# Kernel optimization log

Hardware: AMD Instinct MI355X
Metric: run time of the kernel (lower is better)

## Reference

```python
import jax, jax.numpy as jnp
import numpy as np

BS, NA, HW, C, HEADS = 16, 256, 1024, 512, 8
FEAT_RES = 32  # hw = feat_res**2


def setup_inputs() -> dict:
    key = jax.random.key(0)
    ks = jax.random.split(key, 16)

    def lin_w(k, din, dout):
        return (jax.random.normal(k, (din, dout), jnp.float32) / np.sqrt(din)).astype(jnp.float32)

    inp = {
        "tok_agent": jax.random.normal(ks[0], (BS, NA, C), jnp.float32),
        "enc_feat_supp": jax.random.normal(ks[1], (BS, HW, C), jnp.float32),
        "enc_feat_query": jax.random.normal(ks[2], (BS, HW, C), jnp.float32),
        # projection weights stored as [in, out]
        "W_qa": lin_w(ks[3], C, C), "b_qa": jnp.zeros((C,), jnp.float32),
        "W_ks": lin_w(ks[4], C, C), "b_ks": jnp.zeros((C,), jnp.float32),
        "W_ka": lin_w(ks[5], C, C), "b_ka": jnp.zeros((C,), jnp.float32),
        "W_vs": lin_w(ks[6], C, C), "b_vs": jnp.zeros((C,), jnp.float32),
        # FFN: c -> 3c -> c
        "W_f1": lin_w(ks[7], C, 3 * C), "b_f1": jnp.zeros((3 * C,), jnp.float32),
        "W_f2": lin_w(ks[8], 3 * C, C), "b_f2": jnp.zeros((C,), jnp.float32),
    }
    return inp


def reference(tok_agent, enc_feat_supp, enc_feat_query,
              W_qa, b_qa, W_ks, b_ks, W_ka, b_ka, W_vs, b_vs,
              W_f1, b_f1, W_f2, b_f2):
    bs, na, c = tok_agent.shape
    hw = enc_feat_supp.shape[1]
    feat_res = int(round(np.sqrt(hw)))
    d_k_sqrt = np.float32(np.sqrt(c // HEADS))

    qa = tok_agent @ W_qa + b_qa                 # [bs, na, c]
    ks_ = enc_feat_supp @ W_ks + b_ks            # [bs, hw, c]
    qq = enc_feat_query @ W_qa + b_qa            # NOTE: original reuses qa_linear
    ka = tok_agent @ W_ka + b_ka                 # [bs, na, c]
    vs = enc_feat_supp @ W_vs + b_vs             # [bs, hw, c]

    scores_as = jnp.einsum('bac,bhc->bah', qa, ks_) / d_k_sqrt   # [bs, na, hw]
    scores_qa = jnp.einsum('bhc,bac->bha', qq, ka) / d_k_sqrt    # [bs, hw, na]

    # align_mat[b,i,j] = (argmax_a scores_as[b,a,i] == argmax_a scores_qa[b,j,a])
    a_idx = jnp.argmax(scores_as, axis=1)        # [bs, hw]
    b_idx = jnp.argmax(scores_qa, axis=2)        # [bs, hw]
    align = jnp.where(a_idx[:, :, None] == b_idx[:, None, :],
                      jnp.float32(0.0), jnp.float32(-1e6))       # [bs, hw, hw]

    # scores_sa @ scores_aq: [bs,hw,na] @ [bs,na,hw]
    logits = jnp.einsum('bai,bja->bij', scores_as, scores_qa)    # [bs, hw, hw]
    scores_qs = jax.nn.softmax(logits + align, axis=-1)

    # scores_qs^T @ vs : out[b,j,c] = sum_i scores_qs[b,i,j] * vs[b,i,c]
    dec = jnp.einsum('bij,bic->bjc', scores_qs, vs)              # [bs, hw, c]
    dec = jax.nn.relu(dec @ W_f1 + b_f1) @ W_f2 + b_f2           # FFN (dropout = eval identity)

    # raw memory reinterpretation, as in torch .view
    return dec.reshape(bs, c, feat_res, -1)
```

## Files before the change

### kernel.cpp

```cpp
#include <hip/hip_runtime.h>

typedef float          f32x4  __attribute__((ext_vector_type(4)));
typedef short          bf16x8 __attribute__((ext_vector_type(8)));
typedef _Float16       f16x8  __attribute__((ext_vector_type(8)));
typedef unsigned short u16x4  __attribute__((ext_vector_type(4)));

static constexpr int kBS = 16;
static constexpr int kHW = 1024;

__device__ __forceinline__ unsigned short f2bf(float x) {
  union { float f; unsigned int u; } v; v.f = x;
  unsigned int r = v.u + 0x7fffu + ((v.u >> 16) & 1u);
  return (unsigned short)(r >> 16);
}
__device__ __forceinline__ float bf2f(unsigned short h) {
  union { unsigned int u; float f; } v; v.u = ((unsigned int)h) << 16;
  return v.f;
}
__device__ __forceinline__ unsigned short h2u(_Float16 h) {
  union { _Float16 h; unsigned short u; } v; v.h = h; return v.u;
}

__device__ __forceinline__ void split2h(float x, unsigned short& u0, unsigned short& u1) {
  _Float16 h0 = (_Float16)x;
  if (fabsf(x) < 6.1035156e-05f) h0 = (_Float16)0.f;
  const float r = (x - (float)h0) * 4096.f;
  u0 = h2u(h0);
  u1 = h2u((_Float16)r);
}

__global__ __launch_bounds__(256)
void split_act2h(const f32x4* __restrict__ X, u16x4* __restrict__ P0,
                 u16x4* __restrict__ P1, int n4)
{
  int i = blockIdx.x * 256 + threadIdx.x;
  if (i >= n4) return;
  f32x4 x = X[i];
  u16x4 s0, s1;
#pragma unroll
  for (int u = 0; u < 4; ++u) {
    unsigned short a, b;
    split2h(x[u], a, b);
    s0[u] = a; s1[u] = b;
  }
  P0[i] = s0; P1[i] = s1;
}

__global__ __launch_bounds__(256)
void split_wT2h(const float* __restrict__ Wm, unsigned short* __restrict__ T0,
                unsigned short* __restrict__ T1, int K, int N)
{
  __shared__ float ts[32][33];
  const int k0 = blockIdx.x * 32, n0 = blockIdx.y * 32;
  const int tx = threadIdx.x, ty = threadIdx.y;
#pragma unroll
  for (int r = 0; r < 4; ++r)
    ts[ty + r * 8][tx] = Wm[(size_t)(k0 + ty + r * 8) * N + n0 + tx];
  __syncthreads();
#pragma unroll
  for (int r = 0; r < 4; ++r) {
    const int n = ty + r * 8;
    const size_t off = (size_t)(n0 + n) * K + k0 + tx;
    unsigned short a, b;
    split2h(ts[tx][n], a, b);
    T0[off] = a; T1[off] = b;
  }
}

template<bool F16>
__global__ __launch_bounds__(256)
void split_wT1(const float* __restrict__ Wm, unsigned short* __restrict__ T0,
               int K, int N)
{
  __shared__ float ts[32][33];
  const int k0 = blockIdx.x * 32, n0 = blockIdx.y * 32;
  const int tx = threadIdx.x, ty = threadIdx.y;
#pragma unroll
  for (int r = 0; r < 4; ++r)
    ts[ty + r * 8][tx] = Wm[(size_t)(k0 + ty + r * 8) * N + n0 + tx];
  __syncthreads();
#pragma unroll
  for (int r = 0; r < 4; ++r) {
    const int n = ty + r * 8;
    const float x = ts[tx][n];
    const size_t off = (size_t)(n0 + n) * K + k0 + tx;
    T0[off] = F16 ? h2u((_Float16)x) : f2bf(x);
  }
}

__device__ __forceinline__ void stage_tile(const unsigned short* src, int K,
                                           unsigned short* ldst, int wv, int lane)
{
#pragma unroll
  for (int i = 0; i < 2; ++i) {
    const int s   = wv * 128 + i * 64 + lane;
    const int row = s >> 2;
    const int gc  = ((s & 3) ^ ((row >> 1) & 3)) * 8;
    __builtin_amdgcn_global_load_lds(
        (const __attribute__((address_space(1))) void*)(src + (size_t)row * K + gc),
        (__attribute__((address_space(3))) void*)(ldst + ((wv * 128 + i * 64) << 3)),
        16, 0, 0);
  }
}

template<int OUTM, bool BIAS>
__global__ __launch_bounds__(256)
void gmph(const unsigned short* __restrict__ A0, const unsigned short* __restrict__ A1,
          const unsigned short* __restrict__ B0, const unsigned short* __restrict__ B1,
          const float* __restrict__ bias,
          float* __restrict__ Cf, unsigned short* __restrict__ O0,
          unsigned short* __restrict__ O1,
          int K, int ldc, long sA, long sB, long sC, long sBias, float scale)
{
  __shared__ alignas(16) unsigned short lds[4 * 4096];

  const int tid  = threadIdx.x;
  const int wv   = tid >> 6, lane = tid & 63;
  const int wr   = wv >> 1,  wc   = wv & 1;
  const int cr   = lane & 15, cg  = lane >> 4;
  const int bm   = blockIdx.x * 128, bn = blockIdx.y * 128;

  const size_t zA = (size_t)blockIdx.z * (size_t)sA;
  const size_t zB = (size_t)blockIdx.z * (size_t)sB;
  const size_t zC = (size_t)blockIdx.z * (size_t)sC;
  const size_t zBias = (size_t)blockIdx.z * (size_t)sBias;

  const unsigned short* srcs[4];
  srcs[0] = A0 + zA + (size_t)bm * K;
  srcs[1] = A1 + zA + (size_t)bm * K;
  srcs[2] = B0 + zB + (size_t)bn * K;
  srcs[3] = B1 + zB + (size_t)bn * K;

  f32x4 acc0[4][4], acc1[4][4];
#pragma unroll
  for (int i = 0; i < 4; ++i)
#pragma unroll
    for (int j = 0; j < 4; ++j)
#pragma unroll
      for (int r = 0; r < 4; ++r) { acc0[i][j][r] = 0.f; acc1[i][j][r] = 0.f; }

#define LOADA(pa)                                                               \
  {                                                                             \
    _Pragma("unroll")                                                           \
    for (int f = 0; f < 4; ++f) {                                               \
      const int ra = wr * 64 + f * 16 + cr;                                     \
      af[f] = *(const f16x8*)&lds[(pa) * 4096 + (ra * 4 + (cg ^ ((ra >> 1) & 3))) * 8]; \
    }                                                                           \
  }
#define DOPB(pb, ACC)                                                           \
  {                                                                             \
    f16x8 bfr[4];                                                               \
    _Pragma("unroll")                                                           \
    for (int f = 0; f < 4; ++f) {                                               \
      const int rb = wc * 64 + f * 16 + cr;                                     \
      bfr[f] = *(const f16x8*)&lds[(2 + (pb)) * 4096 + (rb * 4 + (cg ^ ((rb >> 1) & 3))) * 8]; \
    }                                                                           \
    _Pragma("unroll")                                                           \
    for (int i = 0; i < 4; ++i)                                                 \
      _Pragma("unroll")                                                         \
      for (int j = 0; j < 4; ++j)                                               \
        ACC[i][j] = __builtin_amdgcn_mfma_f32_16x16x32_f16(af[i], bfr[j], ACC[i][j], 0, 0, 0); \
  }

  const int nt = K >> 5;
  for (int kt = 0; kt < nt; ++kt) {
    if (kt) __syncthreads();
#pragma unroll
    for (int t = 0; t < 4; ++t)
      stage_tile(srcs[t] + kt * 32, K, &lds[t * 4096], wv, lane);
    __syncthreads();
    f16x8 af[4];
    LOADA(0); DOPB(0, acc0); DOPB(1, acc1);
    LOADA(1); DOPB(0, acc1);
  }
#undef LOADA
#undef DOPB

  const float RS = 2.44140625e-4f;
  float* CfB = Cf + zC;
  unsigned short* O0B = O0 + zC;
  unsigned short* O1B = O1 + zC;
#pragma unroll
  for (int fm = 0; fm < 4; ++fm) {
#pragma unroll
    for (int fn = 0; fn < 4; ++fn) {
      const int n  = bn + wc * 64 + fn * 16 + cr;
      const int m0 = bm + wr * 64 + fm * 16 + 4 * cg;
      float bv = 0.f;
      if (BIAS) bv = bias[zBias + n];
#pragma unroll
      for (int r = 0; r < 4; ++r) {
        const float x = (acc0[fm][fn][r] + acc1[fm][fn][r] * RS) * scale + bv;
        const size_t off = (size_t)(m0 + r) * ldc + n;
        if (OUTM == 0) CfB[off] = x;
        else {
          unsigned short a, b;
          split2h(x, a, b);
          O0B[off] = a; O1B[off] = b;
          if (OUTM == 2) CfB[off] = x;
        }
      }
    }
  }
}

template<int OUTM, bool BIAS, bool RELU, bool F16>
__global__ __launch_bounds__(256)
void gmfma(const unsigned short* __restrict__ A0, const unsigned short* __restrict__ B0,
           const float* __restrict__ bias,
           float* __restrict__ Cf, unsigned short* __restrict__ O0,
           int K, int ldc, long sA, long sB, long sC, float scale)
{
  __shared__ alignas(16) unsigned short lsA[2][4096];
  __shared__ alignas(16) unsigned short lsB[2][4096];

  const int tid  = threadIdx.x;
  const int wv   = tid >> 6, lane = tid & 63;
  const int wr   = wv >> 1,  wc   = wv & 1;
  const int cr   = lane & 15, cg  = lane >> 4;
  const int bm   = blockIdx.x * 128, bn = blockIdx.y * 128;

  const unsigned short* Ap = A0 + (size_t)blockIdx.z * (size_t)sA + (size_t)bm * K;
  const unsigned short* Bp = B0 + (size_t)blockIdx.z * (size_t)sB + (size_t)bn * K;
  const size_t zC = (size_t)blockIdx.z * (size_t)sC;

  f32x4 acc[4][4];
#pragma unroll
  for (int i = 0; i < 4; ++i)
#pragma unroll
    for (int j = 0; j < 4; ++j)
#pragma unroll
      for (int r = 0; r < 4; ++r) acc[i][j][r] = 0.f;

  const int nt = K >> 5;
  stage_tile(Ap, K, lsA[0], wv, lane);
  stage_tile(Bp, K, lsB[0], wv, lane);
  for (int t = 0; t < nt; ++t) {
    __syncthreads();
    const int tn = t + 1;
    if (tn < nt) {
      stage_tile(Ap + tn * 32, K, lsA[tn & 1], wv, lane);
      stage_tile(Bp + tn * 32, K, lsB[tn & 1], wv, lane);
    }
    const unsigned short* lA = lsA[t & 1];
    const unsigned short* lB = lsB[t & 1];
    bf16x8 af[4], bf[4];
#pragma unroll
    for (int f = 0; f < 4; ++f) {
      const int ra = wr * 64 + f * 16 + cr;
      af[f] = *(const bf16x8*)&lA[(ra * 4 + (cg ^ ((ra >> 1) & 3))) * 8];
      const int rb = wc * 64 + f * 16 + cr;
      bf[f] = *(const bf16x8*)&lB[(rb * 4 + (cg ^ ((rb >> 1) & 3))) * 8];
    }
#pragma unroll
    for (int i = 0; i < 4; ++i)
#pragma unroll
      for (int j = 0; j < 4; ++j) {
        if (F16)
          acc[i][j] = __builtin_amdgcn_mfma_f32_16x16x32_f16(
              __builtin_bit_cast(f16x8, af[i]), __builtin_bit_cast(f16x8, bf[j]),
              acc[i][j], 0, 0, 0);
        else
          acc[i][j] = __builtin_amdgcn_mfma_f32_16x16x32_bf16(af[i], bf[j], acc[i][j], 0, 0, 0);
      }
  }

  float* CfB = Cf + zC;
  unsigned short* O0B = O0 + zC;
#pragma unroll
  for (int fm = 0; fm < 4; ++fm) {
#pragma unroll
    for (int fn = 0; fn < 4; ++fn) {
      const int n  = bn + wc * 64 + fn * 16 + cr;
      const int m0 = bm + wr * 64 + fm * 16 + 4 * cg;
      float bv = 0.f;
      if (BIAS) bv = bias[n];
      f32x4 v = acc[fm][fn];
      if (OUTM == 2) {
        u16x4 o;
#pragma unroll
        for (int r = 0; r < 4; ++r) {
          float x = v[r] * scale + bv;
          if (RELU) x = fmaxf(x, 0.f);
          o[r] = f2bf(x);
        }
        *(u16x4*)(O0B + (size_t)n * ldc + m0) = o;
      } else {
#pragma unroll
        for (int r = 0; r < 4; ++r) {
          float x = v[r] * scale + bv;
          if (RELU) x = fmaxf(x, 0.f);
          const size_t off = (size_t)(m0 + r) * ldc + n;
          if (OUTM == 0) CfB[off] = x;
          else O0B[off] = f2bf(x);
        }
      }
    }
  }
}

__global__ __launch_bounds__(256)
void row_argmax4(const float* __restrict__ X, int* __restrict__ out)
{
  const int row = blockIdx.x * 4 + (threadIdx.x >> 6);
  const float* xr = X + (size_t)row * 256;
  const int lane = threadIdx.x & 63;
  float best = -3.0e38f;
  int bi = 0;
#pragma unroll
  for (int t = 0; t < 4; ++t) {
    const int a = lane + (t << 6);
    const float x = xr[a];
    if (x > best) { best = x; bi = a; }
  }
#pragma unroll
  for (int off = 32; off >= 1; off >>= 1) {
    const float ov = __shfl_xor(best, off);
    const int   oi = __shfl_xor(bi, off);
    if (ov > best || (ov == best && oi < bi)) { best = ov; bi = oi; }
  }
  if (lane == 0) out[row] = bi;
}

__global__ __launch_bounds__(256)
void softmax_T(const float* __restrict__ Lg, const int* __restrict__ aidx,
               const int* __restrict__ bidx, unsigned short* __restrict__ PT,
               int ihalf)
{
  __shared__ int bj[1024];
  __shared__ unsigned short tile[1024 * 17];
  const int tid = threadIdx.x;
  const int i0  = blockIdx.x * 16;
  const int b   = blockIdx.y;
  const int r   = tid >> 4;
  const int l16 = tid & 15;

  for (int j = tid; j < 1024; j += 256) bj[j] = bidx[(b << 10) + j];
  __syncthreads();

  const int ai  = aidx[(b << 10) + (ihalf << 9) + i0 + r];
  const float* Lr = Lg + ((size_t)b * 512 + i0 + r) * 1024;
  const int jb = l16 * 64;

  float x[64];
  float mx = -3.0e38f;
#pragma unroll
  for (int q = 0; q < 16; ++q) {
    f32x4 f = *(const f32x4*)(Lr + jb + (q << 2));
#pragma unroll
    for (int u = 0; u < 4; ++u) {
      const int j = jb + (q << 2) + u;
      float t = f[u];
      if (bj[j] != ai) t -= 1e6f;
      x[(q << 2) + u] = t;
      mx = fmaxf(mx, t);
    }
  }
#pragma unroll
  for (int off = 8; off >= 1; off >>= 1) mx = fmaxf(mx, __shfl_xor(mx, off));
  float s = 0.f;
#pragma unroll
  for (int k = 0; k < 64; ++k) { float e = expf(x[k] - mx); x[k] = e; s += e; }
#pragma unroll
  for (int off = 8; off >= 1; off >>= 1) s += __shfl_xor(s, off);
  const float inv = 1.f / s;

#pragma unroll
  for (int k = 0; k < 64; ++k)
    tile[(jb + k) * 17 + r] = f2bf(x[k] * inv);
  __syncthreads();

  for (int j = tid; j < 1024; j += 256) {
    const unsigned short* tp = &tile[j * 17];
    unsigned int w[8];
#pragma unroll
    for (int q = 0; q < 8; ++q)
      w[q] = (unsigned int)tp[2 * q] | ((unsigned int)tp[2 * q + 1] << 16);
    const size_t off = ((size_t)b << 20) + ((size_t)j << 10) + (ihalf << 9) + i0;
    unsigned int* dst = (unsigned int*)(PT + off);
    *(uint4*)dst       = make_uint4(w[0], w[1], w[2], w[3]);
    *((uint4*)dst + 1) = make_uint4(w[4], w[5], w[6], w[7]);
  }
}

extern "C" void kernel_launch(void* const* d_in, const int* in_sizes, int n_in,
                              void* d_out, int out_size, void* d_ws, size_t ws_size,
                              hipStream_t stream)
{
  (void)in_sizes; (void)n_in; (void)out_size; (void)ws_size;

  const float* tok  = (const float*)d_in[0];
  const float* supp = (const float*)d_in[1];
  const float* qry  = (const float*)d_in[2];
  const float* W_qa = (const float*)d_in[3];
  const float* b_qa = (const float*)d_in[4];
  const float* W_ks = (const float*)d_in[5];
  const float* b_ks = (const float*)d_in[6];
  const float* W_ka = (const float*)d_in[7];
  const float* b_ka = (const float*)d_in[8];
  const float* W_vs = (const float*)d_in[9];
  const float* b_vs = (const float*)d_in[10];
  const float* W_f1 = (const float*)d_in[11];
  const float* b_f1 = (const float*)d_in[12];
  const float* W_f2 = (const float*)d_in[13];
  const float* b_f2 = (const float*)d_in[14];

  char* W = (char*)d_ws;
  constexpr size_t MiB = 1048576;
  auto U = [&](double off) { return (unsigned short*)(W + (size_t)(off * MiB)); };
  auto F = [&](double off) { return (float*)(W + (size_t)(off * MiB)); };
  auto I = [&](double off) { return (int*)(W + (size_t)(off * MiB)); };

  const double oTOK0=0, oTOK1=4, oQTF=0, oSUP0=0, oSAF=0, oPT=0;
  const double oWQAT=16, oWKAT=17.5, oWKST=19, oWVST=20.5;
  const double oQA0=22, oQA1=26, oDEC=32, oKA0=34, oKA1=38;
  const double oQRY0=46, oQRY1=62, oQTP0=46, oQTP1=54;
  const double oSUP1=62, oVST=62, oSAP0=78, oSAP1=86;
  const double oQQ0=94, oQQ1=110, oLG=94, oMID=62;
  const double oWF1=142, oWF2=143.5, oBIA=148, oIDXB=150, oIDXA=150.0625;
  const double hP = 0.5;

  const dim3 B256(256), BW(32, 8);
  float* dummyF = F(oLG);
  unsigned short* dummyU = U(oLG);

  hipMemcpyAsync(W + (size_t)(oBIA * MiB), b_qa, 2048, hipMemcpyDeviceToDevice, stream);
  hipMemcpyAsync(W + (size_t)(oBIA * MiB) + 2048, b_ka, 2048, hipMemcpyDeviceToDevice, stream);

  split_wT2h<<<dim3(16,16), BW, 0, stream>>>(W_qa, U(oWQAT), U(oWQAT+hP), 512, 512);
  split_wT2h<<<dim3(16,16), BW, 0, stream>>>(W_ka, U(oWKAT), U(oWKAT+hP), 512, 512);
  split_wT2h<<<dim3(16,16), BW, 0, stream>>>(W_ks, U(oWKST), U(oWKST+hP), 512, 512);
  split_wT1<true><<<dim3(16,16), BW, 0, stream>>>(W_vs, U(oWVST), 512, 512);
  split_act2h<<<dim3(2048), B256, 0, stream>>>((const f32x4*)tok, (u16x4*)U(oTOK0), (u16x4*)U(oTOK1), 524288);
  gmph<1,true><<<dim3(32,4,2), B256, 0, stream>>>(
      U(oTOK0),U(oTOK1), U(oWQAT),U(oWQAT+hP),
      F(oBIA), dummyF, U(oQA0),U(oQA1), 512, 512, 0, 786432, 6291456, 512, 1.f);
  split_act2h<<<dim3(8192), B256, 0, stream>>>((const f32x4*)qry, (u16x4*)U(oQRY0), (u16x4*)U(oQRY1), 2097152);
  gmph<1,true><<<dim3(128,4,1), B256, 0, stream>>>(
      U(oQRY0),U(oQRY1), U(oWQAT),U(oWQAT+hP),
      b_qa, dummyF, U(oQQ0),U(oQQ1), 512, 512, 0,0,0,0, 1.f);
  gmph<2,false><<<dim3(8,2,16), B256, 0, stream>>>(
      U(oQQ0),U(oQQ1), U(oKA0),U(oKA1),
      nullptr, F(oQTF), U(oQTP0),U(oQTP1), 512, 256,
      524288, 131072, 262144, 0, 0.125f);
  row_argmax4<<<dim3(kBS * kHW / 4), B256, 0, stream>>>(F(oQTF), I(oIDXB));
  split_act2h<<<dim3(8192), B256, 0, stream>>>((const f32x4*)supp, (u16x4*)U(oSUP0), (u16x4*)U(oSUP1), 2097152);
  gmph<1,true><<<dim3(128,4,1), B256, 0, stream>>>(
      U(oSUP0),U(oSUP1), U(oWKST),U(oWKST+hP),
      b_ks, dummyF, U(oQQ0),U(oQQ1), 512, 512, 0,0,0,0, 1.f);
  gmfma<2,true,false,true><<<dim3(8,4,16), B256, 0, stream>>>(
      U(oSUP0), U(oWVST), b_vs, dummyF, U(oVST), 512, 1024,
      524288, 0, 524288, 1.f);
  gmph<2,false><<<dim3(8,2,16), B256, 0, stream>>>(
      U(oQQ0),U(oQQ1), U(oQA0),U(oQA1),
      nullptr, F(oSAF), U(oSAP0),U(oSAP1), 512, 256,
      524288, 131072, 262144, 0, 0.125f);
  row_argmax4<<<dim3(kBS * kHW / 4), B256, 0, stream>>>(F(oSAF), I(oIDXA));
  split_wT1<false><<<dim3(16,48), BW, 0, stream>>>(W_f1, U(oWF1), 512, 1536);
  split_wT1<false><<<dim3(48,16), BW, 0, stream>>>(W_f2, U(oWF2), 1536, 512);
  for (int h = 0; h < 2; ++h) {
    gmph<0,false><<<dim3(4,8,16), B256, 0, stream>>>(
        U(oSAP0) + (size_t)h*512*256, U(oSAP1) + (size_t)h*512*256,
        U(oQTP0), U(oQTP1),
        nullptr, F(oLG), dummyU,dummyU, 256, 1024,
        262144, 262144, 524288, 0, 1.f);
    softmax_T<<<dim3(32,16), B256, 0, stream>>>(F(oLG), I(oIDXA), I(oIDXB), U(oPT), h);
  }
  gmfma<1,false,false,false><<<dim3(8,4,16), B256, 0, stream>>>(
      U(oPT), U(oVST), nullptr, dummyF, U(oDEC), 1024, 512,
      1048576, 524288, 524288, 1.f);
  gmfma<1,true,true,false><<<dim3(128,12,1), B256, 0, stream>>>(
      U(oDEC), U(oWF1), b_f1, dummyF, U(oMID), 512, 1536, 0,0,0, 1.f);
  gmfma<0,true,false,false><<<dim3(128,4,1), B256, 0, stream>>>(
      U(oMID), U(oWF2), b_f2, (float*)d_out, dummyU, 1536, 512, 0,0,0, 1.f);
}
```

Measured before the change: 452.2 us.

## Unify GEMM kernels into one template with K-unrolled staging and double-buffering

After: 432.4 us. -4.4%, faster.

```diff
diff --git a/kernel.cpp b/kernel.cpp
--- a/kernel.cpp
+++ b/kernel.cpp
@@ -103,16 +103,20 @@
   }
 }
 
-template<int OUTM, bool BIAS>
-__global__ __launch_bounds__(256)
-void gmph(const unsigned short* __restrict__ A0, const unsigned short* __restrict__ A1,
-          const unsigned short* __restrict__ B0, const unsigned short* __restrict__ B1,
-          const float* __restrict__ bias,
-          float* __restrict__ Cf, unsigned short* __restrict__ O0,
-          unsigned short* __restrict__ O1,
-          int K, int ldc, long sA, long sB, long sC, long sBias, float scale)
-{
-  __shared__ alignas(16) unsigned short lds[4 * 4096];
+template<int ORD, int KU, bool DBUF, int OUTM, bool BIAS, bool RELU, bool F16IN>
+__global__ __launch_bounds__(256)
+void gke(const unsigned short* __restrict__ A0, const unsigned short* __restrict__ A1,
+         const unsigned short* __restrict__ B0, const unsigned short* __restrict__ B1,
+         const float* __restrict__ bias,
+         float* __restrict__ Cf, unsigned short* __restrict__ O0,
+         unsigned short* __restrict__ O1,
+         int K, int ldc, long sA, long sB, long sC, long sBias, float scale)
+{
+  constexpr int NP  = ORD + 1;
+  constexpr int NT  = 2 * NP;
+  constexpr int TPP = KU * NT;
+  static_assert(!DBUF || TPP * 2 == 16, "vmcnt constant assumes 16 loads/phase");
+  extern __shared__ __align__(16) unsigned short lds[];
 
   const int tid  = threadIdx.x;
   const int wv   = tid >> 6, lane = tid & 63;
@@ -125,11 +129,11 @@
   const size_t zC = (size_t)blockIdx.z * (size_t)sC;
   const size_t zBias = (size_t)blockIdx.z * (size_t)sBias;
 
-  const unsigned short* srcs[4];
+  const unsigned short* srcs[NT];
   srcs[0] = A0 + zA + (size_t)bm * K;
-  srcs[1] = A1 + zA + (size_t)bm * K;
-  srcs[2] = B0 + zB + (size_t)bn * K;
-  srcs[3] = B1 + zB + (size_t)bn * K;
+  if (NP == 2) srcs[1] = A1 + zA + (size_t)bm * K;
+  srcs[NP + 0] = B0 + zB + (size_t)bn * K;
+  if (NP == 2) srcs[NP + 1] = B1 + zB + (size_t)bn * K;
 
   f32x4 acc0[4][4], acc1[4][4];
 #pragma unroll
@@ -137,44 +141,92 @@
 #pragma unroll
     for (int j = 0; j < 4; ++j)
 #pragma unroll
-      for (int r = 0; r < 4; ++r) { acc0[i][j][r] = 0.f; acc1[i][j][r] = 0.f; }
-
-#define LOADA(pa)                                                               \
+      for (int r = 0; r < 4; ++r) {
+        acc0[i][j][r] = 0.f;
+        if (ORD == 1) acc1[i][j][r] = 0.f;
+      }
+
+#define STAGE_PH(ph, buf)                                                       \
+  {                                                                             \
+    _Pragma("unroll")                                                           \
+    for (int u = 0; u < KU; ++u)                                                \
+      _Pragma("unroll")                                                         \
+      for (int t = 0; t < NT; ++t)                                              \
+        stage_tile(srcs[t] + ((ph) * KU + u) * 32, K,                           \
+                   lds + (size_t)((buf) * TPP + u * NT + t) * 4096, wv, lane);  \
+  }
+#define LOADA(u, pa)                                                            \
   {                                                                             \
     _Pragma("unroll")                                                           \
     for (int f = 0; f < 4; ++f) {                                               \
       const int ra = wr * 64 + f * 16 + cr;                                     \
-      af[f] = *(const f16x8*)&lds[(pa) * 4096 + (ra * 4 + (cg ^ ((ra >> 1) & 3))) * 8]; \
+      af[f] = *(const bf16x8*)&lb[(size_t)((u) * NT + (pa)) * 4096 +            \
+                                  (ra * 4 + (cg ^ ((ra >> 1) & 3))) * 8];       \
     }                                                                           \
   }
-#define DOPB(pb, ACC)                                                           \
+#define DOPB(u, pb, ACC)                                                        \
   {                                                                             \
-    f16x8 bfr[4];                                                               \
+    bf16x8 bfr[4];                                                              \
     _Pragma("unroll")                                                           \
     for (int f = 0; f < 4; ++f) {                                               \
       const int rb = wc * 64 + f * 16 + cr;                                     \
-      bfr[f] = *(const f16x8*)&lds[(2 + (pb)) * 4096 + (rb * 4 + (cg ^ ((rb >> 1) & 3))) * 8]; \
+      bfr[f] = *(const bf16x8*)&lb[(size_t)((u) * NT + NP + (pb)) * 4096 +      \
+                                   (rb * 4 + (cg ^ ((rb >> 1) & 3))) * 8];      \
     }                                                                           \
     _Pragma("unroll")                                                           \
     for (int i = 0; i < 4; ++i)                                                 \
       _Pragma("unroll")                                                         \
-      for (int j = 0; j < 4; ++j)                                               \
-        ACC[i][j] = __builtin_amdgcn_mfma_f32_16x16x32_f16(af[i], bfr[j], ACC[i][j], 0, 0, 0); \
-  }
-
-  const int nt = K >> 5;
-  for (int kt = 0; kt < nt; ++kt) {
-    if (kt) __syncthreads();
-#pragma unroll
-    for (int t = 0; t < 4; ++t)
-      stage_tile(srcs[t] + kt * 32, K, &lds[t * 4096], wv, lane);
-    __syncthreads();
-    f16x8 af[4];
-    LOADA(0); DOPB(0, acc0); DOPB(1, acc1);
-    LOADA(1); DOPB(0, acc1);
-  }
+      for (int j = 0; j < 4; ++j) {                                             \
+        if constexpr (F16IN)                                                    \
+          ACC[i][j] = __builtin_amdgcn_mfma_f32_16x16x32_f16(                   \
+              __builtin_bit_cast(f16x8, af[i]), __builtin_bit_cast(f16x8, bfr[j]), \
+              ACC[i][j], 0, 0, 0);                                              \
+        else                                                                    \
+          ACC[i][j] = __builtin_amdgcn_mfma_f32_16x16x32_bf16(af[i], bfr[j],    \
+              ACC[i][j], 0, 0, 0);                                              \
+      }                                                                         \
+  }
+#define COMPUTE_PH(buf)                                                         \
+  {                                                                             \
+    const unsigned short* lb = lds + (size_t)(buf) * TPP * 4096;                \
+    bf16x8 af[4];                                                               \
+    _Pragma("unroll")                                                           \
+    for (int u = 0; u < KU; ++u) {                                              \
+      if constexpr (ORD == 1) {                                                 \
+        LOADA(u, 0); DOPB(u, 0, acc0); DOPB(u, 1, acc1);                        \
+        LOADA(u, 1); DOPB(u, 0, acc1);                                          \
+      } else {                                                                  \
+        LOADA(u, 0); DOPB(u, 0, acc0);                                          \
+      }                                                                         \
+    }                                                                           \
+  }
+
+  const int nph = K / (32 * KU);
+  if constexpr (!DBUF) {
+    for (int ph = 0; ph < nph; ++ph) {
+      if (ph) __syncthreads();
+      STAGE_PH(ph, 0);
+      __syncthreads();
+      COMPUTE_PH(0);
+    }
+  } else {
+    STAGE_PH(0, 0);
+    STAGE_PH(1, 1);
+    for (int ph = 0; ph < nph; ++ph) {
+      if (ph + 1 < nph) asm volatile("s_waitcnt vmcnt(16)" ::: "memory");
+      else              asm volatile("s_waitcnt vmcnt(0)" ::: "memory");
+      __builtin_amdgcn_sched_barrier(0);
+      __builtin_amdgcn_s_barrier();
+      COMPUTE_PH(ph & 1);
+      __builtin_amdgcn_s_barrier();
+      __builtin_amdgcn_sched_barrier(0);
+      if (ph + 2 < nph) STAGE_PH(ph + 2, ph & 1);
+    }
+  }
+#undef STAGE_PH
 #undef LOADA
 #undef DOPB
+#undef COMPUTE_PH
 
   const float RS = 2.44140625e-4f;
   float* CfB = Cf + zC;
@@ -188,99 +240,13 @@
       const int m0 = bm + wr * 64 + fm * 16 + 4 * cg;
       float bv = 0.f;
       if (BIAS) bv = bias[zBias + n];
-#pragma unroll
-      for (int r = 0; r < 4; ++r) {
-        const float x = (acc0[fm][fn][r] + acc1[fm][fn][r] * RS) * scale + bv;
-        const size_t off = (size_t)(m0 + r) * ldc + n;
-        if (OUTM == 0) CfB[off] = x;
-        else {
-          unsigned short a, b;
-          split2h(x, a, b);
-          O0B[off] = a; O1B[off] = b;
-          if (OUTM == 2) CfB[off] = x;
-        }
-      }
-    }
-  }
-}
-
-template<int OUTM, bool BIAS, bool RELU, bool F16>
-__global__ __launch_bounds__(256)
-void gmfma(const unsigned short* __restrict__ A0, const unsigned short* __restrict__ B0,
-           const float* __restrict__ bias,
-           float* __restrict__ Cf, unsigned short* __restrict__ O0,
-           int K, int ldc, long sA, long sB, long sC, float scale)
-{
-  __shared__ alignas(16) unsigned short lsA[2][4096];
-  __shared__ alignas(16) unsigned short lsB[2][4096];
-
-  const int tid  = threadIdx.x;
-  const int wv   = tid >> 6, lane = tid & 63;
-  const int wr   = wv >> 1,  wc   = wv & 1;
-  const int cr   = lane & 15, cg  = lane >> 4;
-  const int bm   = blockIdx.x * 128, bn = blockIdx.y * 128;
-
-  const unsigned short* Ap = A0 + (size_t)blockIdx.z * (size_t)sA + (size_t)bm * K;
-  const unsigned short* Bp = B0 + (size_t)blockIdx.z * (size_t)sB + (size_t)bn * K;
-  const size_t zC = (size_t)blockIdx.z * (size_t)sC;
-
-  f32x4 acc[4][4];
-#pragma unroll
-  for (int i = 0; i < 4; ++i)
-#pragma unroll
-    for (int j = 0; j < 4; ++j)
-#pragma unroll
-      for (int r = 0; r < 4; ++r) acc[i][j][r] = 0.f;
-
-  const int nt = K >> 5;
-  stage_tile(Ap, K, lsA[0], wv, lane);
-  stage_tile(Bp, K, lsB[0], wv, lane);
-  for (int t = 0; t < nt; ++t) {
-    __syncthreads();
-    const int tn = t + 1;
-    if (tn < nt) {
-      stage_tile(Ap + tn * 32, K, lsA[tn & 1], wv, lane);
-      stage_tile(Bp + tn * 32, K, lsB[tn & 1], wv, lane);
-    }
-    const unsigned short* lA = lsA[t & 1];
-    const unsigned short* lB = lsB[t & 1];
-    bf16x8 af[4], bf[4];
-#pragma unroll
-    for (int f = 0; f < 4; ++f) {
-      const int ra = wr * 64 + f * 16 + cr;
-      af[f] = *(const bf16x8*)&lA[(ra * 4 + (cg ^ ((ra >> 1) & 3))) * 8];
-      const int rb = wc * 64 + f * 16 + cr;
-      bf[f] = *(const bf16x8*)&lB[(rb * 4 + (cg ^ ((rb >> 1) & 3))) * 8];
-    }
-#pragma unroll
-    for (int i = 0; i < 4; ++i)
-#pragma unroll
-      for (int j = 0; j < 4; ++j) {
-        if (F16)
-          acc[i][j] = __builtin_amdgcn_mfma_f32_16x16x32_f16(
-              __builtin_bit_cast(f16x8, af[i]), __builtin_bit_cast(f16x8, bf[j]),
-              acc[i][j], 0, 0, 0);
-        else
-          acc[i][j] = __builtin_amdgcn_mfma_f32_16x16x32_bf16(af[i], bf[j], acc[i][j], 0, 0, 0);
-      }
-  }
-
-  float* CfB = Cf + zC;
-  unsigned short* O0B = O0 + zC;
-#pragma unroll
-  for (int fm = 0; fm < 4; ++fm) {
-#pragma unroll
-    for (int fn = 0; fn < 4; ++fn) {
-      const int n  = bn + wc * 64 + fn * 16 + cr;
-      const int m0 = bm + wr * 64 + fm * 16 + 4 * cg;
-      float bv = 0.f;
-      if (BIAS) bv = bias[n];
-      f32x4 v = acc[fm][fn];
-      if (OUTM == 2) {
+      if (OUTM == 4) {
         u16x4 o;
 #pragma unroll
         for (int r = 0; r < 4; ++r) {
-          float x = v[r] * scale + bv;
+          float x = acc0[fm][fn][r];
+          if constexpr (ORD == 1) x += acc1[fm][fn][r] * RS;
+          x = x * scale + bv;
           if (RELU) x = fmaxf(x, 0.f);
           o[r] = f2bf(x);
         }
@@ -288,11 +254,19 @@
       } else {
 #pragma unroll
         for (int r = 0; r < 4; ++r) {
-          float x = v[r] * scale + bv;
+          float x = acc0[fm][fn][r];
+          if constexpr (ORD == 1) x += acc1[fm][fn][r] * RS;
+          x = x * scale + bv;
           if (RELU) x = fmaxf(x, 0.f);
           const size_t off = (size_t)(m0 + r) * ldc + n;
           if (OUTM == 0) CfB[off] = x;
-          else O0B[off] = f2bf(x);
+          else if (OUTM == 3) O0B[off] = f2bf(x);
+          else {
+            unsigned short a, b;
+            split2h(x, a, b);
+            O0B[off] = a; O1B[off] = b;
+            if (OUTM == 2) CfB[off] = x;
+          }
         }
       }
     }
@@ -405,6 +379,21 @@
   const float* W_f2 = (const float*)d_in[13];
   const float* b_f2 = (const float*)d_in[14];
 
+  auto kProj  = &gke<1,2,false,1,true ,false,true >;
+  auto kScore = &gke<1,2,true ,2,false,false,true >;
+  auto kLogit = &gke<1,2,false,0,false,false,true >;
+  auto kVsT   = &gke<0,4,false,4,true ,false,true >;
+  auto kPV    = &gke<0,4,false,3,false,false,false>;
+  auto kFFN1  = &gke<0,4,false,3,true ,true ,false>;
+  auto kFFN2  = &gke<0,4,false,0,true ,false,false>;
+  hipFuncSetAttribute((const void*)kProj,  hipFuncAttributeMaxDynamicSharedMemorySize, 65536);
+  hipFuncSetAttribute((const void*)kScore, hipFuncAttributeMaxDynamicSharedMemorySize, 131072);
+  hipFuncSetAttribute((const void*)kLogit, hipFuncAttributeMaxDynamicSharedMemorySize, 65536);
+  hipFuncSetAttribute((const void*)kVsT,   hipFuncAttributeMaxDynamicSharedMemorySize, 65536);
+  hipFuncSetAttribute((const void*)kPV,    hipFuncAttributeMaxDynamicSharedMemorySize, 65536);
+  hipFuncSetAttribute((const void*)kFFN1,  hipFuncAttributeMaxDynamicSharedMemorySize, 65536);
+  hipFuncSetAttribute((const void*)kFFN2,  hipFuncAttributeMaxDynamicSharedMemorySize, 65536);
+
   char* W = (char*)d_ws;
   constexpr size_t MiB = 1048576;
   auto U = [&](double off) { return (unsigned short*)(W + (size_t)(off * MiB)); };
@@ -432,26 +421,27 @@
   split_wT2h<<<dim3(16,16), BW, 0, stream>>>(W_ks, U(oWKST), U(oWKST+hP), 512, 512);
   split_wT1<true><<<dim3(16,16), BW, 0, stream>>>(W_vs, U(oWVST), 512, 512);
   split_act2h<<<dim3(2048), B256, 0, stream>>>((const f32x4*)tok, (u16x4*)U(oTOK0), (u16x4*)U(oTOK1), 524288);
-  gmph<1,true><<<dim3(32,4,2), B256, 0, stream>>>(
+  kProj<<<dim3(32,4,2), B256, 65536, stream>>>(
       U(oTOK0),U(oTOK1), U(oWQAT),U(oWQAT+hP),
       F(oBIA), dummyF, U(oQA0),U(oQA1), 512, 512, 0, 786432, 6291456, 512, 1.f);
   split_act2h<<<dim3(8192), B256, 0, stream>>>((const f32x4*)qry, (u16x4*)U(oQRY0), (u16x4*)U(oQRY1), 2097152);
-  gmph<1,true><<<dim3(128,4,1), B256, 0, stream>>>(
+  kProj<<<dim3(128,4,1), B256, 65536, stream>>>(
       U(oQRY0),U(oQRY1), U(oWQAT),U(oWQAT+hP),
       b_qa, dummyF, U(oQQ0),U(oQQ1), 512, 512, 0,0,0,0, 1.f);
-  gmph<2,false><<<dim3(8,2,16), B256, 0, stream>>>(
+  kScore<<<dim3(8,2,16), B256, 131072, stream>>>(
       U(oQQ0),U(oQQ1), U(oKA0),U(oKA1),
       nullptr, F(oQTF), U(oQTP0),U(oQTP1), 512, 256,
       524288, 131072, 262144, 0, 0.125f);
   row_argmax4<<<dim3(kBS * kHW / 4), B256, 0, stream>>>(F(oQTF), I(oIDXB));
   split_act2h<<<dim3(8192), B256, 0, stream>>>((const f32x4*)supp, (u16x4*)U(oSUP0), (u16x4*)U(oSUP1), 2097152);
-  gmph<1,true><<<dim3(128,4,1), B256, 0, stream>>>(
+  kProj<<<dim3(128,4,1), B256, 65536, stream>>>(
       U(oSUP0),U(oSUP1), U(oWKST),U(oWKST+hP),
       b_ks, dummyF, U(oQQ0),U(oQQ1), 512, 512, 0,0,0,0, 1.f);
-  gmfma<2,true,false,true><<<dim3(8,4,16), B256, 0, stream>>>(
-      U(oSUP0), U(oWVST), b_vs, dummyF, U(oVST), 512, 1024,
-      524288, 0, 524288, 1.f);
-  gmph<2,false><<<dim3(8,2,16), B256, 0, stream>>>(
+  kVsT<<<dim3(8,4,16), B256, 65536, stream>>>(
+      U(oSUP0),dummyU, U(oWVST),dummyU,
+      b_vs, dummyF, U(oVST),dummyU, 512, 1024,
+      524288, 0, 524288, 0, 1.f);
+  kScore<<<dim3(8,2,16), B256, 131072, stream>>>(
       U(oQQ0),U(oQQ1), U(oQA0),U(oQA1),
       nullptr, F(oSAF), U(oSAP0),U(oSAP1), 512, 256,
       524288, 131072, 262144, 0, 0.125f);
@@ -459,18 +449,21 @@
   split_wT1<false><<<dim3(16,48), BW, 0, stream>>>(W_f1, U(oWF1), 512, 1536);
   split_wT1<false><<<dim3(48,16), BW, 0, stream>>>(W_f2, U(oWF2), 1536, 512);
   for (int h = 0; h < 2; ++h) {
-    gmph<0,false><<<dim3(4,8,16), B256, 0, stream>>>(
+    kLogit<<<dim3(4,8,16), B256, 65536, stream>>>(
         U(oSAP0) + (size_t)h*512*256, U(oSAP1) + (size_t)h*512*256,
         U(oQTP0), U(oQTP1),
         nullptr, F(oLG), dummyU,dummyU, 256, 1024,
         262144, 262144, 524288, 0, 1.f);
     softmax_T<<<dim3(32,16), B256, 0, stream>>>(F(oLG), I(oIDXA), I(oIDXB), U(oPT), h);
   }
-  gmfma<1,false,false,false><<<dim3(8,4,16), B256, 0, stream>>>(
-      U(oPT), U(oVST), nullptr, dummyF, U(oDEC), 1024, 512,
-      1048576, 524288, 524288, 1.f);
-  gmfma<1,true,true,false><<<dim3(128,12,1), B256, 0, stream>>>(
-      U(oDEC), U(oWF1), b_f1, dummyF, U(oMID), 512, 1536, 0,0,0, 1.f);
-  gmfma<0,true,false,false><<<dim3(128,4,1), B256, 0, stream>>>(
-      U(oMID), U(oWF2), b_f2, (float*)d_out, dummyU, 1536, 512, 0,0,0, 1.f);
-}
+  kPV<<<dim3(8,4,16), B256, 65536, stream>>>(
+      U(oPT),dummyU, U(oVST),dummyU,
+      nullptr, dummyF, U(oDEC),dummyU, 1024, 512,
+      1048576, 524288, 524288, 0, 1.f);
+  kFFN1<<<dim3(128,12,1), B256, 65536, stream>>>(
+      U(oDEC),dummyU, U(oWF1),dummyU,
+      b_f1, dummyF, U(oMID),dummyU, 512, 1536, 0,0,0,0, 1.f);
+  kFFN2<<<dim3(128,4,1), B256, 65536, stream>>>(
+      U(oMID),dummyU, U(oWF2),dummyU,
+      b_f2, (float*)d_out, dummyU,dummyU, 1536, 512, 0,0,0,0, 1.f);
+}
```
